# Optimization experiments

Hardware: AMD Instinct MI355X
Metric: run time of the kernel (lower is better)

The kernel has to match this reference:

```python
import jax, jax.numpy as jnp
import numpy as np

BN_EPS = 1e-5

def _conv1x1(x, w, b):
    # x: [B,C,H,W], w: [O,C], b: [O]
    return jnp.einsum('bchw,oc->bohw', x, w) + b[None, :, None, None]

def _maxpool2x2(x):
    B, C, H, W = x.shape
    return x.reshape(B, C, H // 2, 2, W // 2, 2).max(axis=(3, 5))

def setup_inputs() -> dict:
    key = jax.random.key(0)
    ks = jax.random.split(key, 6)
    B, C, H, W = 8, 256, 64, 64
    Ci = C // 2  # inter_channels default
    x = jax.random.normal(ks[0], (B, C, H, W), jnp.float32)
    s = lambda k, sh: jax.random.normal(k, sh, jnp.float32) * 0.02
    return {
        'x': x,
        'w_g': s(ks[1], (Ci, C)), 'b_g': jnp.zeros((Ci,), jnp.float32),
        'w_theta': s(ks[2], (Ci, C)), 'b_theta': jnp.zeros((Ci,), jnp.float32),
        'w_phi': s(ks[3], (Ci, C)), 'b_phi': jnp.zeros((Ci,), jnp.float32),
        'w_w': s(ks[4], (C, Ci)), 'b_w': jnp.zeros((C,), jnp.float32),
        'bn_gamma': 1.0 + 0.1 * jax.random.normal(ks[5], (C,), jnp.float32),
        'bn_beta': jnp.zeros((C,), jnp.float32),
    }

def reference(x, w_g, b_g, w_theta, b_theta, w_phi, b_phi, w_w, b_w, bn_gamma, bn_beta):
    B, C, H, W = x.shape
    Ci = w_g.shape[0]
    # projections (sub_sample=True: maxpool 2x2 on g and phi)
    g_x = _maxpool2x2(_conv1x1(x, w_g, b_g)).reshape(B, Ci, -1)          # [B,Ci,M]
    g_x = g_x.transpose(0, 2, 1)                                          # [B,M,Ci]
    theta_x = _conv1x1(x, w_theta, b_theta).reshape(B, Ci, -1)            # [B,Ci,N]
    theta_x = theta_x.transpose(0, 2, 1)                                  # [B,N,Ci]
    phi_x = _maxpool2x2(_conv1x1(x, w_phi, b_phi)).reshape(B, Ci, -1)     # [B,Ci,M]
    # unscaled embedded-Gaussian attention (no 1/sqrt(d), as in source)
    f = jnp.einsum('bnc,bcm->bnm', theta_x, phi_x)                        # [B,N,M]
    f_div_C = jax.nn.softmax(f, axis=-1)
    y = jnp.einsum('bnm,bmc->bnc', f_div_C, g_x)                          # [B,N,Ci]
    y = y.transpose(0, 2, 1).reshape(B, Ci, H, W)
    # W: 1x1 conv + BatchNorm (training mode: batch statistics)
    wy = _conv1x1(y, w_w, b_w)                                            # [B,C,H,W]
    mean = wy.mean(axis=(0, 2, 3), keepdims=True)
    var = wy.var(axis=(0, 2, 3), keepdims=True)
    wy = (wy - mean) * jax.lax.rsqrt(var + BN_EPS)
    wy = wy * bn_gamma[None, :, None, None] + bn_beta[None, :, None, None]
    return wy + x
```

## Files before the change

### kernel.cpp

```cpp
#include <hip/hip_runtime.h>
#include <hip/hip_bf16.h>

#define NB 8
#define NC 256
#define NCI 128
#define NSP 4096
#define NM 1024

typedef float f32x4 __attribute__((ext_vector_type(4)));
typedef short s16x8 __attribute__((ext_vector_type(8)));
typedef unsigned short u16;

#define OFF_XH  (0ull)
#define OFF_XL  (16777216ull)
#define OFF_THT (33554432ull)
#define OFF_PHT (41943040ull)
#define OFF_GP  (44040192ull)
#define OFF_YH  (46137344ull)
#define OFF_YL  (54525952ull)
#define OFF_WY  (0ull)
#define OFF_WBH (62914560ull)
#define OFF_WBL (63111168ull)
#define OFF_WWH (63307776ull)
#define OFF_WWL (63373312ull)
#define OFF_S   (63438848ull)

__device__ __forceinline__ u16 f2bf(float f) {
  union { __hip_bfloat16 h; u16 u; } v;
  v.h = __float2bfloat16(f);
  return v.u;
}
__device__ __forceinline__ float bf2f(u16 u) {
  union { unsigned u; float f; } v;
  v.u = (unsigned)u << 16;
  return v.f;
}
__device__ __forceinline__ u16 bfmax4(u16 a, u16 b, u16 c, u16 d) {
  float v = fmaxf(fmaxf(bf2f(a), bf2f(b)), fmaxf(bf2f(c), bf2f(d)));
  return f2bf(v);
}

__global__ void zero_stats(float* s) { s[threadIdx.x] = 0.f; }

__global__ __launch_bounds__(256) void wcvt(
    const float* __restrict__ wg, const float* __restrict__ wth,
    const float* __restrict__ wph, const float* __restrict__ ww,
    u16* __restrict__ wbh, u16* __restrict__ wbl,
    u16* __restrict__ wwh, u16* __restrict__ wwl)
{
  int idx = blockIdx.x * 256 + threadIdx.x;
  if (idx < 384 * 256) {
    int row = idx >> 8, k = idx & 255;
    float v = row < 128 ? wg[row * 256 + k]
            : row < 256 ? wth[(row - 128) * 256 + k]
                        : wph[(row - 256) * 256 + k];
    u16 h = f2bf(v);
    wbh[idx] = h;
    wbl[idx] = f2bf(v - bf2f(h));
  } else {
    int j = idx - 384 * 256;
    float v = ww[j];
    u16 h = f2bf(v);
    wwh[j] = h;
    wwl[j] = f2bf(v - bf2f(h));
  }
}

__global__ __launch_bounds__(256) void xt_cvt(const float* __restrict__ x,
                                              u16* __restrict__ xh, u16* __restrict__ xl)
{
  __shared__ float t[64 * 68];
  const int n0 = blockIdx.x << 6, c0 = blockIdx.y << 6, b = blockIdx.z;
  const int tid = threadIdx.x;
  const int cl = tid >> 4, n4 = (tid & 15) << 2;
#pragma unroll
  for (int it = 0; it < 4; ++it) {
    int c = it * 16 + cl;
    float4 v = *(const float4*)&x[((size_t)(b * NC + c0 + c)) * NSP + n0 + n4];
    *(float4*)&t[c * 68 + n4] = v;
  }
  __syncthreads();
#pragma unroll
  for (int it = 0; it < 2; ++it) {
    int task = it * 256 + tid;
    int n = task >> 3, cc = (task & 7) << 3;
    u16 oh[8], ol[8];
#pragma unroll
    for (int i = 0; i < 8; ++i) {
      float v = t[(cc + i) * 68 + n];
      oh[i] = f2bf(v);
      ol[i] = f2bf(v - bf2f(oh[i]));
    }
    size_t dst = ((size_t)(b * NSP + n0 + n)) * NC + c0 + cc;
    *(s16x8*)&xh[dst] = *(s16x8*)oh;
    *(s16x8*)&xl[dst] = *(s16x8*)ol;
  }
}

__global__ __launch_bounds__(512, 1) void proj_fused(
    const u16* __restrict__ xh, const u16* __restrict__ xl,
    const u16* __restrict__ wbh, const u16* __restrict__ wbl,
    const float* __restrict__ bg, const float* __restrict__ bth,
    const float* __restrict__ bph,
    u16* __restrict__ thT, u16* __restrict__ phT, u16* __restrict__ gp)
{
  __shared__ char smem[132608];
  u16* xsh = (u16*)smem;
  u16* xsl = (u16*)(smem + 16384);
  u16* wsh = (u16*)(smem + 32768);
  u16* wsl = (u16*)(smem + 81920);
  u16* outl = (u16*)smem;
  float* bias = (float*)(smem + 131072);

  const int b = blockIdx.y, h2 = blockIdx.x;
  const int n0 = h2 << 7;
  const int tid = threadIdx.x;
  const int wave = tid >> 6, lane = tid & 63;
  const int lo16 = lane & 15, hi4 = lane >> 4;
  const int wr = wave >> 1, wc = wave & 1;
  const int obase = wr * 96, nbase = wc * 64;

  if (tid < 384)
    bias[tid] = tid < 128 ? bg[tid] : tid < 256 ? bth[tid - 128] : bph[tid - 256];

  f32x4 acc[6][4];
#pragma unroll
  for (int i = 0; i < 6; ++i)
#pragma unroll
    for (int j = 0; j < 4; ++j) acc[i][j] = (f32x4){0.f, 0.f, 0.f, 0.f};

  for (int step = 0; step < 4; ++step) {
    __syncthreads();
#pragma unroll
    for (int i = 0; i < 2; ++i) {
      int ci = i * 512 + tid;
      int n = ci >> 3, slot = ci & 7;
      size_t rowb = ((size_t)(b * NSP + n0 + n)) * 512 + step * 128 + ((slot ^ (n & 7)) << 4);
      char* dsth = (char*)xsh + (size_t)(i * 512 + (tid & ~63)) * 16;
      char* dstl = (char*)xsl + (size_t)(i * 512 + (tid & ~63)) * 16;
      __builtin_amdgcn_global_load_lds((const __attribute__((address_space(1))) unsigned*)((const char*)xh + rowb),
                                       (__attribute__((address_space(3))) unsigned*)dsth, 16, 0, 0);
      __builtin_amdgcn_global_load_lds((const __attribute__((address_space(1))) unsigned*)((const char*)xl + rowb),
                                       (__attribute__((address_space(3))) unsigned*)dstl, 16, 0, 0);
    }
#pragma unroll
    for (int i = 0; i < 6; ++i) {
      int ci = i * 512 + tid;
      int o = ci >> 3, slot = ci & 7;
      size_t rowb = (size_t)o * 512 + step * 128 + ((slot ^ (o & 7)) << 4);
      char* dsth = (char*)wsh + (size_t)(i * 512 + (tid & ~63)) * 16;
      char* dstl = (char*)wsl + (size_t)(i * 512 + (tid & ~63)) * 16;
      __builtin_amdgcn_global_load_lds((const __attribute__((address_space(1))) unsigned*)((const char*)wbh + rowb),
                                       (__attribute__((address_space(3))) unsigned*)dsth, 16, 0, 0);
      __builtin_amdgcn_global_load_lds((const __attribute__((address_space(1))) unsigned*)((const char*)wbl + rowb),
                                       (__attribute__((address_space(3))) unsigned*)dstl, 16, 0, 0);
    }
    __syncthreads();

#pragma unroll
    for (int kc = 0; kc < 2; ++kc) {
      const int sl = kc * 4 + hi4;
      s16x8 bfh[4], bfl[4];
#pragma unroll
      for (int fn = 0; fn < 4; ++fn) {
        int n = nbase + fn * 16 + lo16;
        int off = (int)n * 128 + ((sl ^ (n & 7)) << 4);
        bfh[fn] = *(const s16x8*)((const char*)xsh + off);
        bfl[fn] = *(const s16x8*)((const char*)xsl + off);
      }
#pragma unroll
      for (int fo = 0; fo < 6; ++fo) {
        int o = obase + fo * 16 + lo16;
        int off = (int)o * 128 + ((sl ^ (o & 7)) << 4);
        s16x8 afh = *(const s16x8*)((const char*)wsh + off);
        s16x8 afl = *(const s16x8*)((const char*)wsl + off);
#pragma unroll
        for (int fn = 0; fn < 4; ++fn) {
          acc[fo][fn] = __builtin_amdgcn_mfma_f32_16x16x32_bf16(afh, bfh[fn], acc[fo][fn], 0, 0, 0);
          acc[fo][fn] = __builtin_amdgcn_mfma_f32_16x16x32_bf16(afh, bfl[fn], acc[fo][fn], 0, 0, 0);
          acc[fo][fn] = __builtin_amdgcn_mfma_f32_16x16x32_bf16(afl, bfh[fn], acc[fo][fn], 0, 0, 0);
        }
      }
    }
  }

  __syncthreads();
#pragma unroll
  for (int fo = 0; fo < 6; ++fo) {
    int orow = obase + fo * 16 + hi4 * 4;
    f32x4 bv = *(const f32x4*)&bias[orow];
#pragma unroll
    for (int fn = 0; fn < 4; ++fn) {
      int n = nbase + fn * 16 + lo16;
#pragma unroll
      for (int r = 0; r < 4; ++r)
        outl[(orow + r) * 137 + n] = f2bf(acc[fo][fn][r] + bv[r]);
    }
  }
  __syncthreads();

#pragma unroll
  for (int it = 0; it < 4; ++it) {
    int task = it * 512 + tid;
    int n = task >> 4, cc = (task & 15) << 3;
    u16 o[8];
#pragma unroll
    for (int i = 0; i < 8; ++i) o[i] = outl[(128 + cc + i) * 137 + n];
    *(s16x8*)&thT[((size_t)(b * NSP + n0 + n)) * NCI + cc] = *(s16x8*)o;
  }
  {
    int c = tid >> 2, wq = tid & 3;
    u16 o[8];
#pragma unroll
    for (int j = 0; j < 8; ++j) {
      int w2 = wq * 8 + j;
      o[j] = bfmax4(outl[c * 137 + 2 * w2], outl[c * 137 + 2 * w2 + 1],
                    outl[c * 137 + 64 + 2 * w2], outl[c * 137 + 64 + 2 * w2 + 1]);
    }
    *(s16x8*)&gp[((size_t)(b * NCI + c)) * NM + (h2 << 5) + wq * 8] = *(s16x8*)o;
  }
  {
    int w2 = tid >> 4, cc = (tid & 15) << 3;
    u16 o[8];
#pragma unroll
    for (int i = 0; i < 8; ++i) {
      int c = 256 + cc + i;
      o[i] = bfmax4(outl[c * 137 + 2 * w2], outl[c * 137 + 2 * w2 + 1],
                    outl[c * 137 + 64 + 2 * w2], outl[c * 137 + 64 + 2 * w2 + 1]);
    }
    *(s16x8*)&phT[((size_t)(b * NM + (h2 << 5) + w2)) * NCI + cc] = *(s16x8*)o;
  }
}

__global__ __launch_bounds__(512, 1) void attn_mfma(
    const u16* __restrict__ thT, const u16* __restrict__ phT,
    const u16* __restrict__ gP, u16* __restrict__ yh, u16* __restrict__ yl)
{
  __shared__ u16 phs[64 * 128];
  __shared__ u16 gs[128 * 64];
  __shared__ u16 ps[8][16 * 72];

  const int b = blockIdx.y;
  const int n0 = blockIdx.x << 7;
  const int tid = threadIdx.x;
  const int wave = tid >> 6;
  const int lane = tid & 63;
  const int lo16 = lane & 15;
  const int hi4 = lane >> 4;
  const int qbase = n0 + (wave << 4);
  const int swq = (lo16 & 7) << 4;

  s16x8 tha[4];
#pragma unroll
  for (int kc = 0; kc < 4; ++kc)
    tha[kc] = *(const s16x8*)&thT[((size_t)b * NSP + qbase + lo16) * NCI + kc * 32 + hi4 * 8];

  f32x4 yacc[8];
#pragma unroll
  for (int i = 0; i < 8; ++i) yacc[i] = (f32x4){0.f, 0.f, 0.f, 0.f};
  float m_i[4] = {-3e38f, -3e38f, -3e38f, -3e38f};
  float l_i[4] = {0.f, 0.f, 0.f, 0.f};

  for (int mt = 0; mt < 16; ++mt) {
    const int m0 = mt << 6;
    __syncthreads();
#pragma unroll
    for (int i = 0; i < 2; ++i) {
      int ofs = (i * 512 + tid) * 16;
      int m = ofs >> 8, cb = ofs & 255;
      const char* src = (const char*)phT + (((size_t)b * NM + m0 + m) << 8) + (cb ^ ((m & 7) << 4));
      char* dst = (char*)phs + (size_t)(i * 512 + (tid & ~63)) * 16;
      __builtin_amdgcn_global_load_lds((const __attribute__((address_space(1))) unsigned*)src,
                                       (__attribute__((address_space(3))) unsigned*)dst, 16, 0, 0);
    }
#pragma unroll
    for (int i = 0; i < 2; ++i) {
      int ofs = (i * 512 + tid) * 16;
      int c = ofs >> 7, mb = ofs & 127;
      const char* src = (const char*)gP + (((size_t)b * NCI + c) << 11) + m0 * 2 + (mb ^ ((c & 7) << 4));
      char* dst = (char*)gs + (size_t)(i * 512 + (tid & ~63)) * 16;
      __builtin_amdgcn_global_load_lds((const __attribute__((address_space(1))) unsigned*)src,
                                       (__attribute__((address_space(3))) unsigned*)dst, 16, 0, 0);
    }
    __syncthreads();

    f32x4 sf[4];
#pragma unroll
    for (int ms = 0; ms < 4; ++ms) sf[ms] = (f32x4){0.f, 0.f, 0.f, 0.f};
#pragma unroll
    for (int ms = 0; ms < 4; ++ms) {
      const int rbase = (ms * 16 + lo16) << 8;
#pragma unroll
      for (int kc = 0; kc < 4; ++kc) {
        s16x8 bp = *(const s16x8*)((const char*)phs + rbase + ((kc * 64 + hi4 * 16) ^ swq));
        sf[ms] = __builtin_amdgcn_mfma_f32_16x16x32_bf16(tha[kc], bp, sf[ms], 0, 0, 0);
      }
    }

    float scv[4];
#pragma unroll
    for (int r = 0; r < 4; ++r) {
      float v = fmaxf(fmaxf(sf[0][r], sf[1][r]), fmaxf(sf[2][r], sf[3][r]));
      v = fmaxf(v, __shfl_xor(v, 1));
      v = fmaxf(v, __shfl_xor(v, 2));
      v = fmaxf(v, __shfl_xor(v, 4));
      v = fmaxf(v, __shfl_xor(v, 8));
      float mn = fmaxf(m_i[r], v);
      float sc = __expf(m_i[r] - mn);
      float rs = 0.f;
#pragma unroll
      for (int ms = 0; ms < 4; ++ms) {
        float e = __expf(sf[ms][r] - mn);
        sf[ms][r] = e;
        rs += e;
      }
      rs += __shfl_xor(rs, 1);
      rs += __shfl_xor(rs, 2);
      rs += __shfl_xor(rs, 4);
      rs += __shfl_xor(rs, 8);
      l_i[r] = l_i[r] * sc + rs;
      m_i[r] = mn;
      scv[r] = sc;
    }
#pragma unroll
    for (int ct = 0; ct < 8; ++ct)
#pragma unroll
      for (int r = 0; r < 4; ++r) yacc[ct][r] *= scv[r];

    u16* pw = ps[wave];
#pragma unroll
    for (int ms = 0; ms < 4; ++ms)
#pragma unroll
      for (int r = 0; r < 4; ++r)
        pw[(hi4 * 4 + r) * 72 + ms * 16 + lo16] = f2bf(sf[ms][r]);
    asm volatile("s_waitcnt lgkmcnt(0)" ::: "memory");

    s16x8 pa[2];
#pragma unroll
    for (int km = 0; km < 2; ++km)
      pa[km] = *(const s16x8*)((const char*)pw + lo16 * 144 + km * 64 + hi4 * 16);

#pragma unroll
    for (int ct = 0; ct < 8; ++ct) {
      const int rb = (ct * 16 + lo16) << 7;
#pragma unroll
      for (int km = 0; km < 2; ++km) {
        s16x8 bg = *(const s16x8*)((const char*)gs + rb + ((km * 64 + hi4 * 16) ^ swq));
        yacc[ct] = __builtin_amdgcn_mfma_f32_16x16x32_bf16(pa[km], bg, yacc[ct], 0, 0, 0);
      }
    }
  }

#pragma unroll
  for (int r = 0; r < 4; ++r) {
    float inv = 1.f / l_i[r];
    size_t row = ((size_t)b * NSP + qbase + hi4 * 4 + r) * NCI;
#pragma unroll
    for (int ct = 0; ct < 8; ++ct) {
      float v = yacc[ct][r] * inv;
      u16 h = f2bf(v);
      yh[row + ct * 16 + lo16] = h;
      yl[row + ct * 16 + lo16] = f2bf(v - bf2f(h));
    }
  }
}

__global__ __launch_bounds__(512, 1) void conv_w_mfma(
    const u16* __restrict__ yh, const u16* __restrict__ yl,
    const u16* __restrict__ wwh, const u16* __restrict__ wwl,
    const float* __restrict__ bw, float* __restrict__ wy,
    float* __restrict__ s1g, float* __restrict__ s2g)
{
  __shared__ char smem[102400];
  u16* wsh = (u16*)smem;
  u16* wsl = (u16*)(smem + 32768);
  u16* ysh = (u16*)(smem + 65536);
  u16* ysl = (u16*)(smem + 81920);
  float (*sums1)[256] = (float(*)[256])(smem + 98304);
  float (*sums2)[256] = (float(*)[256])(smem + 100352);

  const int b = blockIdx.y, n0 = blockIdx.x << 7;
  const int tid = threadIdx.x;
  const int wave = tid >> 6, lane = tid & 63;
  const int lo16 = lane & 15, hi4 = lane >> 4;
  const int wr = wave >> 1, wc = wave & 1;
  const int obase = wr * 64, nbase = wc * 64;

  f32x4 acc[4][4];
#pragma unroll
  for (int i = 0; i < 4; ++i)
#pragma unroll
    for (int j = 0; j < 4; ++j) acc[i][j] = (f32x4){0.f, 0.f, 0.f, 0.f};

  for (int step = 0; step < 2; ++step) {
    __syncthreads();
#pragma unroll
    for (int i = 0; i < 4; ++i) {
      int ci = i * 512 + tid;
      int o = ci >> 3, slot = ci & 7;
      size_t rowb = (size_t)o * 256 + step * 128 + ((slot ^ (o & 7)) << 4);
      char* dsth = (char*)wsh + (size_t)(i * 512 + (tid & ~63)) * 16;
      char* dstl = (char*)wsl + (size_t)(i * 512 + (tid & ~63)) * 16;
      __builtin_amdgcn_global_load_lds((const __attribute__((address_space(1))) unsigned*)((const char*)wwh + rowb),
                                       (__attribute__((address_space(3))) unsigned*)dsth, 16, 0, 0);
      __builtin_amdgcn_global_load_lds((const __attribute__((address_space(1))) unsigned*)((const char*)wwl + rowb),
                                       (__attribute__((address_space(3))) unsigned*)dstl, 16, 0, 0);
    }
#pragma unroll
    for (int i = 0; i < 2; ++i) {
      int ci = i * 512 + tid;
      int n = ci >> 3, slot = ci & 7;
      size_t rowb = ((size_t)(b * NSP + n0 + n)) * 256 + step * 128 + ((slot ^ (n & 7)) << 4);
      char* dsth = (char*)ysh + (size_t)(i * 512 + (tid & ~63)) * 16;
      char* dstl = (char*)ysl + (size_t)(i * 512 + (tid & ~63)) * 16;
      __builtin_amdgcn_global_load_lds((const __attribute__((address_space(1))) unsigned*)((const char*)yh + rowb),
                                       (__attribute__((address_space(3))) unsigned*)dsth, 16, 0, 0);
      __builtin_amdgcn_global_load_lds((const __attribute__((address_space(1))) unsigned*)((const char*)yl + rowb),
                                       (__attribute__((address_space(3))) unsigned*)dstl, 16, 0, 0);
    }
    __syncthreads();

#pragma unroll
    for (int kc = 0; kc < 2; ++kc) {
      const int sl = kc * 4 + hi4;
      s16x8 bfh[4], bfl[4];
#pragma unroll
      for (int fn = 0; fn < 4; ++fn) {
        int n = nbase + fn * 16 + lo16;
        int off = (int)n * 128 + ((sl ^ (n & 7)) << 4);
        bfh[fn] = *(const s16x8*)((const char*)ysh + off);
        bfl[fn] = *(const s16x8*)((const char*)ysl + off);
      }
#pragma unroll
      for (int fo = 0; fo < 4; ++fo) {
        int o = obase + fo * 16 + lo16;
        int off = (int)o * 128 + ((sl ^ (o & 7)) << 4);
        s16x8 afh = *(const s16x8*)((const char*)wsh + off);
        s16x8 afl = *(const s16x8*)((const char*)wsl + off);
#pragma unroll
        for (int fn = 0; fn < 4; ++fn) {
          acc[fo][fn] = __builtin_amdgcn_mfma_f32_16x16x32_bf16(afh, bfh[fn], acc[fo][fn], 0, 0, 0);
          acc[fo][fn] = __builtin_amdgcn_mfma_f32_16x16x32_bf16(afh, bfl[fn], acc[fo][fn], 0, 0, 0);
          acc[fo][fn] = __builtin_amdgcn_mfma_f32_16x16x32_bf16(afl, bfh[fn], acc[fo][fn], 0, 0, 0);
        }
      }
    }
  }

#pragma unroll
  for (int fo = 0; fo < 4; ++fo) {
    int orow = obase + fo * 16 + hi4 * 4;
    float bv[4];
#pragma unroll
    for (int r = 0; r < 4; ++r) bv[r] = bw[orow + r];
    float ss[4] = {0.f, 0.f, 0.f, 0.f}, sq[4] = {0.f, 0.f, 0.f, 0.f};
#pragma unroll
    for (int fn = 0; fn < 4; ++fn) {
      int col = n0 + nbase + fn * 16 + lo16;
#pragma unroll
      for (int r = 0; r < 4; ++r) {
        float v = acc[fo][fn][r] + bv[r];
        wy[((size_t)(b * NC) + orow + r) * NSP + col] = v;
        ss[r] += v;
        sq[r] += v * v;
      }
    }
#pragma unroll
    for (int r = 0; r < 4; ++r) {
#pragma unroll
      for (int d = 1; d < 16; d <<= 1) {
        ss[r] += __shfl_xor(ss[r], d);
        sq[r] += __shfl_xor(sq[r], d);
      }
    }
    if (lo16 == 0) {
#pragma unroll
      for (int r = 0; r < 4; ++r) {
        sums1[wc][orow + r] = ss[r];
        sums2[wc][orow + r] = sq[r];
      }
    }
  }
  __syncthreads();
  if (tid < 256) {
    atomicAdd(&s1g[tid], sums1[0][tid] + sums1[1][tid]);
    atomicAdd(&s2g[tid], sums2[0][tid] + sums2[1][tid]);
  }
}

__global__ __launch_bounds__(256) void bn_res4(
    const float* __restrict__ wy, const float* __restrict__ x,
    const float* __restrict__ s1, const float* __restrict__ s2,
    const float* __restrict__ gamma, const float* __restrict__ beta,
    float* __restrict__ out)
{
  int i4 = (blockIdx.x * 256 + threadIdx.x) << 2;
  int c = (i4 >> 12) & 255;
  const float cnt = 1.f / 32768.f;
  float mean = s1[c] * cnt;
  float var = s2[c] * cnt - mean * mean;
  float inv = rsqrtf(var + 1e-5f) * gamma[c];
  float bet = beta[c];
  float4 w = *(const float4*)&wy[i4];
  float4 xv = *(const float4*)&x[i4];
  float4 o;
  o.x = (w.x - mean) * inv + bet + xv.x;
  o.y = (w.y - mean) * inv + bet + xv.y;
  o.z = (w.z - mean) * inv + bet + xv.z;
  o.w = (w.w - mean) * inv + bet + xv.w;
  *(float4*)&out[i4] = o;
}

extern "C" void kernel_launch(void* const* d_in, const int* in_sizes, int n_in,
                              void* d_out, int out_size, void* d_ws, size_t ws_size,
                              hipStream_t stream) {
  const float* x    = (const float*)d_in[0];
  const float* w_g  = (const float*)d_in[1];
  const float* b_g  = (const float*)d_in[2];
  const float* w_th = (const float*)d_in[3];
  const float* b_th = (const float*)d_in[4];
  const float* w_ph = (const float*)d_in[5];
  const float* b_ph = (const float*)d_in[6];
  const float* w_w  = (const float*)d_in[7];
  const float* b_w  = (const float*)d_in[8];
  const float* gam  = (const float*)d_in[9];
  const float* bet  = (const float*)d_in[10];
  float* out = (float*)d_out;
  char* ws = (char*)d_ws;

  u16*   xh  = (u16*)(ws + OFF_XH);
  u16*   xl  = (u16*)(ws + OFF_XL);
  u16*   thT = (u16*)(ws + OFF_THT);
  u16*   phT = (u16*)(ws + OFF_PHT);
  u16*   gp  = (u16*)(ws + OFF_GP);
  u16*   yhb = (u16*)(ws + OFF_YH);
  u16*   ylb = (u16*)(ws + OFF_YL);
  float* wy  = (float*)(ws + OFF_WY);
  u16*   wbh = (u16*)(ws + OFF_WBH);
  u16*   wbl = (u16*)(ws + OFF_WBL);
  u16*   wwh = (u16*)(ws + OFF_WWH);
  u16*   wwl = (u16*)(ws + OFF_WWL);
  float* s1  = (float*)(ws + OFF_S);
  float* s2  = s1 + 256;

  wcvt<<<dim3(512), 256, 0, stream>>>(w_g, w_th, w_ph, w_w, wbh, wbl, wwh, wwl);
  zero_stats<<<dim3(1), 512, 0, stream>>>(s1);
  xt_cvt<<<dim3(64, 4, 8), 256, 0, stream>>>(x, xh, xl);

  proj_fused<<<dim3(32, 8), 512, 0, stream>>>(xh, xl, wbh, wbl, b_g, b_th, b_ph, thT, phT, gp);

  attn_mfma<<<dim3(32, 8), 512, 0, stream>>>(thT, phT, gp, yhb, ylb);

  conv_w_mfma<<<dim3(32, 8), 512, 0, stream>>>(yhb, ylb, wwh, wwl, b_w, wy, s1, s2);

  bn_res4<<<dim3(8192), 256, 0, stream>>>(wy, x, s1, s2, gam, bet, out);
}
```

Baseline: 129.9 us.

## Double-buffer attention K/V tiles, shrink blocks, and raise MFMA wave priority

The attention kernel now double-buffers the phi and g tiles in shared memory, issuing the next tile's async global-to-LDS loads before computing on the current one. This hides load latency behind the MFMA work. Blocks drop to 256 threads covering 64 queries, and the grid doubles to 512 blocks with two blocks allowed per CU, which raises occupancy and improves balance across CUs. s_setprio is wrapped around the MFMA loops in the projection, attention and output-conv kernels to favour matrix issue. The double buffer doubles LDS use per block, and the synchronisation at the end of each iteration may still serialise part of the work.

```diff
diff --git a/kernel.cpp b/kernel.cpp
--- a/kernel.cpp
+++ b/kernel.cpp
@@ -24,6 +24,10 @@
 #define OFF_WWH (63307776ull)
 #define OFF_WWL (63373312ull)
 #define OFF_S   (63438848ull)
+
+#define GLL(src, dst) __builtin_amdgcn_global_load_lds( \
+    (const __attribute__((address_space(1))) unsigned*)(src), \
+    (__attribute__((address_space(3))) unsigned*)(dst), 16, 0, 0)
 
 __device__ __forceinline__ u16 f2bf(float f) {
   union { __hip_bfloat16 h; u16 u; } v;
@@ -136,24 +140,16 @@
       int ci = i * 512 + tid;
       int n = ci >> 3, slot = ci & 7;
       size_t rowb = ((size_t)(b * NSP + n0 + n)) * 512 + step * 128 + ((slot ^ (n & 7)) << 4);
-      char* dsth = (char*)xsh + (size_t)(i * 512 + (tid & ~63)) * 16;
-      char* dstl = (char*)xsl + (size_t)(i * 512 + (tid & ~63)) * 16;
-      __builtin_amdgcn_global_load_lds((const __attribute__((address_space(1))) unsigned*)((const char*)xh + rowb),
-                                       (__attribute__((address_space(3))) unsigned*)dsth, 16, 0, 0);
-      __builtin_amdgcn_global_load_lds((const __attribute__((address_space(1))) unsigned*)((const char*)xl + rowb),
-                                       (__attribute__((address_space(3))) unsigned*)dstl, 16, 0, 0);
+      GLL((const char*)xh + rowb, (char*)xsh + (size_t)(i * 512 + (tid & ~63)) * 16);
+      GLL((const char*)xl + rowb, (char*)xsl + (size_t)(i * 512 + (tid & ~63)) * 16);
     }
 #pragma unroll
     for (int i = 0; i < 6; ++i) {
       int ci = i * 512 + tid;
       int o = ci >> 3, slot = ci & 7;
       size_t rowb = (size_t)o * 512 + step * 128 + ((slot ^ (o & 7)) << 4);
-      char* dsth = (char*)wsh + (size_t)(i * 512 + (tid & ~63)) * 16;
-      char* dstl = (char*)wsl + (size_t)(i * 512 + (tid & ~63)) * 16;
-      __builtin_amdgcn_global_load_lds((const __attribute__((address_space(1))) unsigned*)((const char*)wbh + rowb),
-                                       (__attribute__((address_space(3))) unsigned*)dsth, 16, 0, 0);
-      __builtin_amdgcn_global_load_lds((const __attribute__((address_space(1))) unsigned*)((const char*)wbl + rowb),
-                                       (__attribute__((address_space(3))) unsigned*)dstl, 16, 0, 0);
+      GLL((const char*)wbh + rowb, (char*)wsh + (size_t)(i * 512 + (tid & ~63)) * 16);
+      GLL((const char*)wbl + rowb, (char*)wsl + (size_t)(i * 512 + (tid & ~63)) * 16);
     }
     __syncthreads();
 
@@ -168,6 +164,7 @@
         bfh[fn] = *(const s16x8*)((const char*)xsh + off);
         bfl[fn] = *(const s16x8*)((const char*)xsl + off);
       }
+      __builtin_amdgcn_s_setprio(1);
 #pragma unroll
       for (int fo = 0; fo < 6; ++fo) {
         int o = obase + fo * 16 + lo16;
@@ -181,6 +178,7 @@
           acc[fo][fn] = __builtin_amdgcn_mfma_f32_16x16x32_bf16(afl, bfh[fn], acc[fo][fn], 0, 0, 0);
         }
       }
+      __builtin_amdgcn_s_setprio(0);
     }
   }
 
@@ -232,16 +230,16 @@
   }
 }
 
-__global__ __launch_bounds__(512, 1) void attn_mfma(
+__global__ __launch_bounds__(256, 2) void attn_mfma(
     const u16* __restrict__ thT, const u16* __restrict__ phT,
     const u16* __restrict__ gP, u16* __restrict__ yh, u16* __restrict__ yl)
 {
-  __shared__ u16 phs[64 * 128];
-  __shared__ u16 gs[128 * 64];
-  __shared__ u16 ps[8][16 * 72];
+  __shared__ u16 phs[2][64 * 128];
+  __shared__ u16 gs[2][128 * 64];
+  __shared__ u16 ps[4][16 * 72];
 
   const int b = blockIdx.y;
-  const int n0 = blockIdx.x << 7;
+  const int n0 = blockIdx.x << 6;
   const int tid = threadIdx.x;
   const int wave = tid >> 6;
   const int lane = tid & 63;
@@ -261,41 +259,47 @@
   float m_i[4] = {-3e38f, -3e38f, -3e38f, -3e38f};
   float l_i[4] = {0.f, 0.f, 0.f, 0.f};
 
+  auto stage = [&](int s, int m0) {
+#pragma unroll
+    for (int i = 0; i < 4; ++i) {
+      int ci = i * 256 + tid;
+      int m = ci >> 4, cb = (ci & 15) << 4;
+      const char* src = (const char*)phT + (((size_t)b * NM + m0 + m) << 8) + (cb ^ ((m & 7) << 4));
+      GLL(src, (char*)phs[s] + (size_t)(i * 256 + (tid & ~63)) * 16);
+    }
+#pragma unroll
+    for (int i = 0; i < 4; ++i) {
+      int ci = i * 256 + tid;
+      int c = ci >> 3, mb = (ci & 7) << 4;
+      const char* src = (const char*)gP + (((size_t)b * NCI + c) << 11) + m0 * 2 + (mb ^ ((c & 7) << 4));
+      GLL(src, (char*)gs[s] + (size_t)(i * 256 + (tid & ~63)) * 16);
+    }
+  };
+
+  stage(0, 0);
+  __syncthreads();
+  int cur = 0;
+
   for (int mt = 0; mt < 16; ++mt) {
-    const int m0 = mt << 6;
-    __syncthreads();
-#pragma unroll
-    for (int i = 0; i < 2; ++i) {
-      int ofs = (i * 512 + tid) * 16;
-      int m = ofs >> 8, cb = ofs & 255;
-      const char* src = (const char*)phT + (((size_t)b * NM + m0 + m) << 8) + (cb ^ ((m & 7) << 4));
-      char* dst = (char*)phs + (size_t)(i * 512 + (tid & ~63)) * 16;
-      __builtin_amdgcn_global_load_lds((const __attribute__((address_space(1))) unsigned*)src,
-                                       (__attribute__((address_space(3))) unsigned*)dst, 16, 0, 0);
-    }
-#pragma unroll
-    for (int i = 0; i < 2; ++i) {
-      int ofs = (i * 512 + tid) * 16;
-      int c = ofs >> 7, mb = ofs & 127;
-      const char* src = (const char*)gP + (((size_t)b * NCI + c) << 11) + m0 * 2 + (mb ^ ((c & 7) << 4));
-      char* dst = (char*)gs + (size_t)(i * 512 + (tid & ~63)) * 16;
-      __builtin_amdgcn_global_load_lds((const __attribute__((address_space(1))) unsigned*)src,
-                                       (__attribute__((address_space(3))) unsigned*)dst, 16, 0, 0);
-    }
-    __syncthreads();
+    if (mt < 15) stage(cur ^ 1, (mt + 1) << 6);
+
+    const u16* ph = phs[cur];
+    const u16* gg = gs[cur];
 
     f32x4 sf[4];
 #pragma unroll
     for (int ms = 0; ms < 4; ++ms) sf[ms] = (f32x4){0.f, 0.f, 0.f, 0.f};
+    __builtin_amdgcn_s_setprio(1);
 #pragma unroll
     for (int ms = 0; ms < 4; ++ms) {
       const int rbase = (ms * 16 + lo16) << 8;
 #pragma unroll
       for (int kc = 0; kc < 4; ++kc) {
-        s16x8 bp = *(const s16x8*)((const char*)phs + rbase + ((kc * 64 + hi4 * 16) ^ swq));
+        s16x8 bp = *(const s16x8*)((const char*)ph + rbase + ((kc * 64 + hi4 * 16) ^ swq));
         sf[ms] = __builtin_amdgcn_mfma_f32_16x16x32_bf16(tha[kc], bp, sf[ms], 0, 0, 0);
       }
     }
+    __builtin_amdgcn_s_setprio(0);
 
     float scv[4];
 #pragma unroll
@@ -340,15 +344,20 @@
     for (int km = 0; km < 2; ++km)
       pa[km] = *(const s16x8*)((const char*)pw + lo16 * 144 + km * 64 + hi4 * 16);
 
+    __builtin_amdgcn_s_setprio(1);
 #pragma unroll
     for (int ct = 0; ct < 8; ++ct) {
       const int rb = (ct * 16 + lo16) << 7;
 #pragma unroll
       for (int km = 0; km < 2; ++km) {
-        s16x8 bg = *(const s16x8*)((const char*)gs + rb + ((km * 64 + hi4 * 16) ^ swq));
+        s16x8 bg = *(const s16x8*)((const char*)gg + rb + ((km * 64 + hi4 * 16) ^ swq));
         yacc[ct] = __builtin_amdgcn_mfma_f32_16x16x32_bf16(pa[km], bg, yacc[ct], 0, 0, 0);
       }
     }
+    __builtin_amdgcn_s_setprio(0);
+
+    __syncthreads();
+    cur ^= 1;
   }
 
 #pragma unroll
@@ -399,24 +408,16 @@
       int ci = i * 512 + tid;
       int o = ci >> 3, slot = ci & 7;
       size_t rowb = (size_t)o * 256 + step * 128 + ((slot ^ (o & 7)) << 4);
-      char* dsth = (char*)wsh + (size_t)(i * 512 + (tid & ~63)) * 16;
-      char* dstl = (char*)wsl + (size_t)(i * 512 + (tid & ~63)) * 16;
-      __builtin_amdgcn_global_load_lds((const __attribute__((address_space(1))) unsigned*)((const char*)wwh + rowb),
-                                       (__attribute__((address_space(3))) unsigned*)dsth, 16, 0, 0);
-      __builtin_amdgcn_global_load_lds((const __attribute__((address_space(1))) unsigned*)((const char*)wwl + rowb),
-                                       (__attribute__((address_space(3))) unsigned*)dstl, 16, 0, 0);
+      GLL((const char*)wwh + rowb, (char*)wsh + (size_t)(i * 512 + (tid & ~63)) * 16);
+      GLL((const char*)wwl + rowb, (char*)wsl + (size_t)(i * 512 + (tid & ~63)) * 16);
     }
 #pragma unroll
     for (int i = 0; i < 2; ++i) {
       int ci = i * 512 + tid;
       int n = ci >> 3, slot = ci & 7;
       size_t rowb = ((size_t)(b * NSP + n0 + n)) * 256 + step * 128 + ((slot ^ (n & 7)) << 4);
-      char* dsth = (char*)ysh + (size_t)(i * 512 + (tid & ~63)) * 16;
-      char* dstl = (char*)ysl + (size_t)(i * 512 + (tid & ~63)) * 16;
-      __builtin_amdgcn_global_load_lds((const __attribute__((address_space(1))) unsigned*)((const char*)yh + rowb),
-                                       (__attribute__((address_space(3))) unsigned*)dsth, 16, 0, 0);
-      __builtin_amdgcn_global_load_lds((const __attribute__((address_space(1))) unsigned*)((const char*)yl + rowb),
-                                       (__attribute__((address_space(3))) unsigned*)dstl, 16, 0, 0);
+      GLL((const char*)yh + rowb, (char*)ysh + (size_t)(i * 512 + (tid & ~63)) * 16);
+      GLL((const char*)yl + rowb, (char*)ysl + (size_t)(i * 512 + (tid & ~63)) * 16);
     }
     __syncthreads();
 
@@ -431,6 +432,7 @@
         bfh[fn] = *(const s16x8*)((const char*)ysh + off);
         bfl[fn] = *(const s16x8*)((const char*)ysl + off);
       }
+      __builtin_amdgcn_s_setprio(1);
 #pragma unroll
       for (int fo = 0; fo < 4; ++fo) {
         int o = obase + fo * 16 + lo16;
@@ -444,6 +446,7 @@
           acc[fo][fn] = __builtin_amdgcn_mfma_f32_16x16x32_bf16(afl, bfh[fn], acc[fo][fn], 0, 0, 0);
         }
       }
+      __builtin_amdgcn_s_setprio(0);
     }
   }
 
@@ -549,7 +552,7 @@
 
   proj_fused<<<dim3(32, 8), 512, 0, stream>>>(xh, xl, wbh, wbl, b_g, b_th, b_ph, thT, phT, gp);
 
-  attn_mfma<<<dim3(32, 8), 512, 0, stream>>>(thT, phT, gp, yhb, ylb);
+  attn_mfma<<<dim3(64, 8), 256, 0, stream>>>(thT, phT, gp, yhb, ylb);
 
   conv_w_mfma<<<dim3(32, 8), 512, 0, stream>>>(yhb, ylb, wwh, wwl, b_w, wy, s1, s2);
 
```

New measurement: 125.7 us. 1.03x faster.
